# Kernel optimization log

Hardware: AMD Instinct MI355X
Metric: run time of the kernel (lower is better)

The kernel has to match this reference:

```python
import jax, jax.numpy as jnp
import numpy as np

N_NODES = 200000
N_EDGES = 6400000


def gcn_conv(x, src, dst, norm, num_nodes, W, b):
    # GCNConv: X' = D^{-1/2} (A+I) D^{-1/2} X W + b
    h = x @ W                                   # [N, out]
    msg = h[src] * norm[:, None]                # gather + scale per edge
    out = jax.ops.segment_sum(msg, dst, num_segments=num_nodes)
    return out + b


def build_norm(edge_index, num_nodes):
    # add self-loops, then symmetric normalization deg^{-1/2}[src]*deg^{-1/2}[dst]
    loops = jnp.arange(num_nodes, dtype=edge_index.dtype)
    src = jnp.concatenate([edge_index[0], loops])
    dst = jnp.concatenate([edge_index[1], loops])
    ones = jnp.ones(src.shape[0], dtype=jnp.float32)
    deg = jax.ops.segment_sum(ones, dst, num_segments=num_nodes)
    dinv = jnp.where(deg > 0, jax.lax.rsqrt(deg), 0.0)
    norm = dinv[src] * dinv[dst]
    return src, dst, norm


def setup_inputs() -> dict:
    key = jax.random.key(0)
    k1, k2, k3, k4 = jax.random.split(key, 4)
    x = jax.random.normal(k1, (N_NODES, 21), dtype=jnp.float32)
    edge_index = jax.random.randint(k2, (2, N_EDGES), 0, N_NODES, dtype=jnp.int64)
    W1 = jax.random.normal(k3, (21, 16), dtype=jnp.float32) * (1.0 / np.sqrt(21))
    b1 = jnp.zeros((16,), dtype=jnp.float32)
    W2 = jax.random.normal(k4, (16, 6), dtype=jnp.float32) * (1.0 / np.sqrt(16))
    b2 = jnp.zeros((6,), dtype=jnp.float32)
    return {"x": x, "edge_index": edge_index, "W1": W1, "b1": b1, "W2": W2, "b2": b2}


def reference(x, edge_index, W1, b1, W2, b2):
    num_nodes = x.shape[0]
    src, dst, norm = build_norm(edge_index, num_nodes)
    h = gcn_conv(x, src, dst, norm, num_nodes, W1, b1)
    h = jax.nn.relu(h)
    # F.dropout with training=self.training: eval mode -> identity
    h = gcn_conv(h, src, dst, norm, num_nodes, W2, b2)
    return jax.nn.log_softmax(h, axis=1)
```

## Files before the change

kernel.cpp:

```cpp
#include <hip/hip_runtime.h>
#include <hip/hip_fp16.h>

#define NFEAT_IN 21
#define NHID 16
#define NOUT 6
#define BSHIFT 9
#define BW (1 << BSHIFT)
#define NB 512
#define PB 256
#define EPT 32
#define CHUNK (PB * EPT)

typedef unsigned int u32x4 __attribute__((ext_vector_type(4)));

__global__ void k_init_bcur(int* __restrict__ bcur, int cap) {
    int b = blockIdx.x * blockDim.x + threadIdx.x;
    if (b < NB) bcur[b] = b * cap;
}

__global__ __launch_bounds__(256) void
k_partition(const int* __restrict__ src, const int* __restrict__ dst,
            int* __restrict__ bcur, unsigned int* __restrict__ bucketed,
            int cap, int ne) {
    __shared__ unsigned int ebd[CHUNK];
    __shared__ unsigned short sidx[CHUNK];
    __shared__ int lcnt[NB], lstart[NB], lcur[NB], lbase[NB];
    __shared__ int s[PB];
    __shared__ int sh_total;
    int t = threadIdx.x;
    long base = (long)blockIdx.x * CHUNK;
    for (int b = t; b < NB; b += PB) lcnt[b] = 0;
    __syncthreads();
#pragma unroll
    for (int k = 0; k < EPT; k++) {
        int idx = t + k * PB;
        long e = base + idx;
        unsigned int v = 0xFFFFFFFFu;
        if (e < ne) {
            int d = dst[e];
            v = (unsigned int)d;
            atomicAdd(&lcnt[d >> BSHIFT], 1);
        }
        ebd[idx] = v;
    }
    __syncthreads();
    int v0 = lcnt[2 * t], v1 = lcnt[2 * t + 1];
    int pair = v0 + v1;
    s[t] = pair;
    __syncthreads();
    for (int off = 1; off < PB; off <<= 1) {
        int tv = (t >= off) ? s[t - off] : 0;
        __syncthreads();
        s[t] += tv;
        __syncthreads();
    }
    int ex = s[t] - pair;
    lstart[2 * t] = ex;          lcur[2 * t] = ex;
    lstart[2 * t + 1] = ex + v0; lcur[2 * t + 1] = ex + v0;
    if (v0 > 0) lbase[2 * t]     = atomicAdd(&bcur[2 * t],     v0);
    if (v1 > 0) lbase[2 * t + 1] = atomicAdd(&bcur[2 * t + 1], v1);
    if (t == PB - 1) sh_total = s[PB - 1];
    __syncthreads();
#pragma unroll
    for (int k = 0; k < EPT; k++) {
        int idx = t + k * PB;
        unsigned int d = ebd[idx];
        if (d != 0xFFFFFFFFu) {
            int r = atomicAdd(&lcur[d >> BSHIFT], 1);
            sidx[r] = (unsigned short)idx;
        }
    }
    __syncthreads();
    int total = sh_total;
#pragma unroll
    for (int k = 0; k < EPT; k++) {
        int j = t + k * PB;
        if (j < total) {
            int idx = sidx[j];
            unsigned int d = ebd[idx];
            int b = d >> BSHIFT;
            long gpos = (long)lbase[b] + (j - lstart[b]);
            int s_ = src[base + idx];
            if (gpos < (long)(b + 1) * cap)
                bucketed[gpos] = ((unsigned int)s_ << BSHIFT) | (d & (BW - 1));
        }
    }
}

__global__ __launch_bounds__(512) void
k_cnt_scan(const int* __restrict__ bcur, int cap, int* __restrict__ cnt,
           int* __restrict__ csr_boff, int nb) {
    __shared__ int s[512];
    int t = threadIdx.x;
    int c = (t < nb) ? (bcur[t] - t * cap) : 0;
    s[t] = c;
    __syncthreads();
    for (int off = 1; off < 512; off <<= 1) {
        int tv = (t >= off) ? s[t - off] : 0;
        __syncthreads();
        s[t] += tv;
        __syncthreads();
    }
    if (t < nb) { cnt[t] = c; csr_boff[t] = s[t] - c; }
}

__global__ __launch_bounds__(512) void
k_sort(const unsigned int* __restrict__ bucketed, int cap,
       const int* __restrict__ cnt, const int* __restrict__ csr_boff,
       int* __restrict__ csr_src, int* __restrict__ node_off,
       float* __restrict__ dinv, int n, int ne, int nb) {
    __shared__ int bin[BW], sc[BW], bcur_l[BW];
    int b = blockIdx.x, t = threadIdx.x;
    bin[t] = 0;
    __syncthreads();
    size_t s0r = (size_t)b * cap;
    int c = cnt[b], s0c = csr_boff[b];
    for (int j = t; j < c; j += 512) atomicAdd(&bin[bucketed[s0r + j] & (BW - 1)], 1);
    __syncthreads();
    sc[t] = bin[t];
    __syncthreads();
    for (int off = 1; off < BW; off <<= 1) {
        int v = (t >= off) ? sc[t - off] : 0;
        __syncthreads();
        sc[t] += v;
        __syncthreads();
    }
    {
        int ex = sc[t] - bin[t];
        bcur_l[t] = s0c + ex;
        node_off[(b << BSHIFT) + t] = s0c + ex;
        int node = (b << BSHIFT) + t;
        if (node < n) dinv[node] = rsqrtf((float)bin[t] + 1.0f);
    }
    if (b == 0 && t == 0) node_off[(size_t)nb << BSHIFT] = ne;
    __syncthreads();
    for (int j = t; j < c; j += 512) {
        unsigned int e = bucketed[s0r + j];
        int pos = atomicAdd(&bcur_l[e & (BW - 1)], 1);
        csr_src[pos] = (int)(e >> BSHIFT);
    }
}

__global__ void k_dense1(const float* __restrict__ x, const float* __restrict__ W1,
                         const float* __restrict__ dinv, __half2* __restrict__ hs1h, int n) {
    __shared__ float sW[NFEAT_IN * NHID];
    for (int t = threadIdx.x; t < NFEAT_IN * NHID; t += blockDim.x) sW[t] = W1[t];
    __syncthreads();
    int i = blockIdx.x * blockDim.x + threadIdx.x;
    if (i >= n) return;
    float xi[NFEAT_IN];
#pragma unroll
    for (int k = 0; k < NFEAT_IN; k++) xi[k] = x[(size_t)i * NFEAT_IN + k];
    float di = dinv[i];
    float r[NHID];
#pragma unroll
    for (int j = 0; j < NHID; j++) {
        float acc = 0.f;
#pragma unroll
        for (int k = 0; k < NFEAT_IN; k++) acc += xi[k] * sW[k * NHID + j];
        r[j] = acc * di;
    }
    __half2* hp = hs1h + (size_t)i * 8;
#pragma unroll
    for (int q = 0; q < 8; q++) hp[q] = __floats2half2_rn(r[2 * q], r[2 * q + 1]);
}

__device__ __forceinline__ void addh16(float* acc, u32x4 u0, u32x4 u1) {
    unsigned int us[8] = {u0[0], u0[1], u0[2], u0[3], u1[0], u1[1], u1[2], u1[3]};
#pragma unroll
    for (int q = 0; q < 8; q++) {
        float2 f = __half22float2(*(const __half2*)&us[q]);
        acc[2 * q] += f.x;
        acc[2 * q + 1] += f.y;
    }
}

__global__ __launch_bounds__(256) void
k_agg1(const int* __restrict__ csr_src, const int* __restrict__ node_off,
       const __half2* __restrict__ hs1h, const float* __restrict__ b1,
       const float* __restrict__ W2, const float* __restrict__ dinv,
       __half2* __restrict__ hs2h, int n) {
    __shared__ float sW[NHID * NOUT];
    __shared__ float sb[NHID];
    int t = threadIdx.x;
    if (t < NHID * NOUT) sW[t] = W2[t];
    if (t < NHID) sb[t] = b1[t];
    __syncthreads();
    int i = blockIdx.x * blockDim.x + t;
    if (i >= n) return;
    int beg = node_off[i], end = node_off[i + 1];
    const u32x4* hb = (const u32x4*)hs1h;
    float acc[NHID];
    {
        u32x4 u0 = hb[(size_t)i * 2], u1 = hb[(size_t)i * 2 + 1];
        unsigned int us[8] = {u0[0], u0[1], u0[2], u0[3], u1[0], u1[1], u1[2], u1[3]};
#pragma unroll
        for (int q = 0; q < 8; q++) {
            float2 f = __half22float2(*(const __half2*)&us[q]);
            acc[2 * q] = f.x;
            acc[2 * q + 1] = f.y;
        }
    }
    int j = beg;
    for (; j + 4 <= end; j += 4) {
        int s0_ = csr_src[j], s1_ = csr_src[j + 1];
        int s2_ = csr_src[j + 2], s3_ = csr_src[j + 3];
        u32x4 a0 = hb[(size_t)s0_ * 2], a1 = hb[(size_t)s0_ * 2 + 1];
        u32x4 b0 = hb[(size_t)s1_ * 2], b1v = hb[(size_t)s1_ * 2 + 1];
        u32x4 c0 = hb[(size_t)s2_ * 2], c1 = hb[(size_t)s2_ * 2 + 1];
        u32x4 d0 = hb[(size_t)s3_ * 2], d1 = hb[(size_t)s3_ * 2 + 1];
        addh16(acc, a0, a1);
        addh16(acc, b0, b1v);
        addh16(acc, c0, c1);
        addh16(acc, d0, d1);
    }
    for (; j < end; j++) {
        int s_ = csr_src[j];
        addh16(acc, hb[(size_t)s_ * 2], hb[(size_t)s_ * 2 + 1]);
    }
    float di = dinv[i];
    float z[NHID];
#pragma unroll
    for (int k = 0; k < NHID; k++) z[k] = fmaxf(acc[k] * di + sb[k], 0.0f);
    float h[8];
#pragma unroll
    for (int kk = 0; kk < NOUT; kk++) {
        float s = 0.f;
#pragma unroll
        for (int jj = 0; jj < NHID; jj++) s += z[jj] * sW[jj * NOUT + kk];
        h[kk] = s * di;
    }
    h[6] = 0.f; h[7] = 0.f;
    __half2* op = hs2h + (size_t)i * 4;
#pragma unroll
    for (int q = 0; q < 4; q++) op[q] = __floats2half2_rn(h[2 * q], h[2 * q + 1]);
}

__global__ __launch_bounds__(256) void
k_agg2(const int* __restrict__ csr_src, const int* __restrict__ node_off,
       const __half2* __restrict__ hs2h, const float* __restrict__ b2,
       const float* __restrict__ dinv, float* __restrict__ out, int n) {
    __shared__ float sb[NOUT];
    int t = threadIdx.x;
    if (t < NOUT) sb[t] = b2[t];
    __syncthreads();
    int i = blockIdx.x * blockDim.x + t;
    if (i >= n) return;
    int beg = node_off[i], end = node_off[i + 1];
    const u32x4* hb = (const u32x4*)hs2h;
    float acc[NOUT];
    {
        u32x4 u = hb[(size_t)i];
        unsigned int us[3] = {u[0], u[1], u[2]};
#pragma unroll
        for (int q = 0; q < 3; q++) {
            float2 f = __half22float2(*(const __half2*)&us[q]);
            acc[2 * q] = f.x;
            acc[2 * q + 1] = f.y;
        }
    }
    int j = beg;
    for (; j + 8 <= end; j += 8) {
        int sid[8];
#pragma unroll
        for (int q = 0; q < 8; q++) sid[q] = csr_src[j + q];
        u32x4 u[8];
#pragma unroll
        for (int q = 0; q < 8; q++) u[q] = hb[(size_t)sid[q]];
#pragma unroll
        for (int q = 0; q < 8; q++) {
            unsigned int us[3] = {u[q][0], u[q][1], u[q][2]};
#pragma unroll
            for (int w = 0; w < 3; w++) {
                float2 fv = __half22float2(*(const __half2*)&us[w]);
                acc[2 * w] += fv.x;
                acc[2 * w + 1] += fv.y;
            }
        }
    }
    for (; j < end; j++) {
        u32x4 u = hb[(size_t)csr_src[j]];
        unsigned int us[3] = {u[0], u[1], u[2]};
#pragma unroll
        for (int w = 0; w < 3; w++) {
            float2 fv = __half22float2(*(const __half2*)&us[w]);
            acc[2 * w] += fv.x;
            acc[2 * w + 1] += fv.y;
        }
    }
    float di = dinv[i];
    float v[NOUT];
#pragma unroll
    for (int k = 0; k < NOUT; k++) v[k] = acc[k] * di + sb[k];
    float m = -1e30f;
#pragma unroll
    for (int k = 0; k < NOUT; k++) m = fmaxf(m, v[k]);
    float se = 0.f;
#pragma unroll
    for (int k = 0; k < NOUT; k++) se += expf(v[k] - m);
    float l = logf(se);
#pragma unroll
    for (int k = 0; k < NOUT; k++) out[(size_t)i * NOUT + k] = v[k] - m - l;
}

extern "C" void kernel_launch(void* const* d_in, const int* in_sizes, int n_in,
                              void* d_out, int out_size, void* d_ws, size_t ws_size,
                              hipStream_t stream) {
    const float* x  = (const float*)d_in[0];
    const int*   ei = (const int*)d_in[1];
    const float* W1 = (const float*)d_in[2];
    const float* b1 = (const float*)d_in[3];
    const float* W2 = (const float*)d_in[4];
    const float* b2 = (const float*)d_in[5];
    float* out = (float*)d_out;

    int n  = in_sizes[0] / NFEAT_IN;
    int ne = in_sizes[1] / 2;
    const int* src = ei;
    const int* dst = ei + ne;

    int nb = (n + BW - 1) >> BSHIFT;
    int cap = (ne + nb - 1) / nb + ne / (nb * 16) + 1536;

    char* base = (char*)d_ws;
    size_t off = 0;
    auto alloc = [&](size_t bytes) {
        void* p = base + off;
        off += (bytes + 63) & ~(size_t)63;
        return p;
    };
    int* bcur     = (int*)alloc(NB * 4);
    int* cnt      = (int*)alloc(NB * 4);
    int* csr_boff = (int*)alloc(NB * 4);
    unsigned int* bucketed = (unsigned int*)alloc((size_t)nb * cap * 4);
    int* csr_src  = (int*)alloc((size_t)ne * 4);
    int* node_off = (int*)alloc(((size_t)nb * BW + 1) * 4);
    float* dinv   = (float*)alloc((size_t)n * 4);
    __half2* hs1h;
    __half2* hs2h;
    if ((size_t)nb * cap * 4 >= (size_t)n * 48) {
        hs1h = (__half2*)bucketed;
        hs2h = (__half2*)((char*)bucketed + (size_t)n * 32);
    } else {
        hs1h = (__half2*)alloc((size_t)n * 32);
        hs2h = (__half2*)alloc((size_t)n * 16);
    }

    int gp = (ne + CHUNK - 1) / CHUNK;
    int gn = (n + 255) / 256;

    k_init_bcur<<<(NB + 255) / 256, 256, 0, stream>>>(bcur, cap);
    k_partition<<<gp, PB, 0, stream>>>(src, dst, bcur, bucketed, cap, ne);
    k_cnt_scan<<<1, 512, 0, stream>>>(bcur, cap, cnt, csr_boff, nb);
    k_sort<<<nb, 512, 0, stream>>>(bucketed, cap, cnt, csr_boff, csr_src, node_off, dinv, n, ne, nb);
    k_dense1<<<gn, 256, 0, stream>>>(x, W1, dinv, hs1h, n);
    k_agg1<<<gn, 256, 0, stream>>>(csr_src, node_off, hs1h, b1, W2, dinv, hs2h, n);
    k_agg2<<<gn, 256, 0, stream>>>(csr_src, node_off, hs2h, b2, dinv, out, n);
}
```

Baseline: 399.5 us.

## Split layer-1 aggregation into two feature-half passes over separate fp16 arrays

The hidden features are stored as two separate 8-wide fp16 arrays (low and high halves), and layer-1 aggregation becomes two kernels, each gathering one 16-byte half per edge. The first pass writes fp32 partial sums, which the second pass reads and combines. The idea is to halve the working set of each gather (3.2MB per half) so it stays cache-resident and random gathers hit more often. The cost is reading the CSR twice, an extra partial-sum round trip and one more launch; CSR index loads are also marked nontemporal.

```diff
diff --git a/kernel.cpp b/kernel.cpp
--- a/kernel.cpp
+++ b/kernel.cpp
@@ -142,7 +142,9 @@
 }
 
 __global__ void k_dense1(const float* __restrict__ x, const float* __restrict__ W1,
-                         const float* __restrict__ dinv, __half2* __restrict__ hs1h, int n) {
+                         const float* __restrict__ dinv,
+                         __half2* __restrict__ hs1lo, __half2* __restrict__ hs1hi,
+                         int n) {
     __shared__ float sW[NFEAT_IN * NHID];
     for (int t = threadIdx.x; t < NFEAT_IN * NHID; t += blockDim.x) sW[t] = W1[t];
     __syncthreads();
@@ -160,15 +162,19 @@
         for (int k = 0; k < NFEAT_IN; k++) acc += xi[k] * sW[k * NHID + j];
         r[j] = acc * di;
     }
-    __half2* hp = hs1h + (size_t)i * 8;
-#pragma unroll
-    for (int q = 0; q < 8; q++) hp[q] = __floats2half2_rn(r[2 * q], r[2 * q + 1]);
-}
-
-__device__ __forceinline__ void addh16(float* acc, u32x4 u0, u32x4 u1) {
-    unsigned int us[8] = {u0[0], u0[1], u0[2], u0[3], u1[0], u1[1], u1[2], u1[3]};
-#pragma unroll
-    for (int q = 0; q < 8; q++) {
+    __half2* lp = hs1lo + (size_t)i * 4;
+    __half2* hp = hs1hi + (size_t)i * 4;
+#pragma unroll
+    for (int q = 0; q < 4; q++) {
+        lp[q] = __floats2half2_rn(r[2 * q], r[2 * q + 1]);
+        hp[q] = __floats2half2_rn(r[8 + 2 * q], r[8 + 2 * q + 1]);
+    }
+}
+
+__device__ __forceinline__ void addh8(float* acc, u32x4 u) {
+    unsigned int us[4] = {u[0], u[1], u[2], u[3]};
+#pragma unroll
+    for (int q = 0; q < 4; q++) {
         float2 f = __half22float2(*(const __half2*)&us[q]);
         acc[2 * q] += f.x;
         acc[2 * q + 1] += f.y;
@@ -176,10 +182,44 @@
 }
 
 __global__ __launch_bounds__(256) void
-k_agg1(const int* __restrict__ csr_src, const int* __restrict__ node_off,
-       const __half2* __restrict__ hs1h, const float* __restrict__ b1,
-       const float* __restrict__ W2, const float* __restrict__ dinv,
-       __half2* __restrict__ hs2h, int n) {
+k_agg1a(const int* __restrict__ csr_src, const int* __restrict__ node_off,
+        const u32x4* __restrict__ hlo, float* __restrict__ pacc, int n) {
+    int i = blockIdx.x * blockDim.x + threadIdx.x;
+    if (i >= n) return;
+    int beg = node_off[i], end = node_off[i + 1];
+    float acc[8];
+    {
+        u32x4 u = hlo[i];
+        unsigned int us[4] = {u[0], u[1], u[2], u[3]};
+#pragma unroll
+        for (int q = 0; q < 4; q++) {
+            float2 f = __half22float2(*(const __half2*)&us[q]);
+            acc[2 * q] = f.x;
+            acc[2 * q + 1] = f.y;
+        }
+    }
+    int j = beg;
+    for (; j + 8 <= end; j += 8) {
+        int sid[8];
+#pragma unroll
+        for (int q = 0; q < 8; q++) sid[q] = __builtin_nontemporal_load(csr_src + j + q);
+        u32x4 u[8];
+#pragma unroll
+        for (int q = 0; q < 8; q++) u[q] = hlo[(size_t)sid[q]];
+#pragma unroll
+        for (int q = 0; q < 8; q++) addh8(acc, u[q]);
+    }
+    for (; j < end; j++) addh8(acc, hlo[(size_t)csr_src[j]]);
+    float4* pp = (float4*)(pacc + (size_t)i * 8);
+    pp[0] = make_float4(acc[0], acc[1], acc[2], acc[3]);
+    pp[1] = make_float4(acc[4], acc[5], acc[6], acc[7]);
+}
+
+__global__ __launch_bounds__(256) void
+k_agg1b(const int* __restrict__ csr_src, const int* __restrict__ node_off,
+        const u32x4* __restrict__ hhi, const float* __restrict__ pacc,
+        const float* __restrict__ b1, const float* __restrict__ W2,
+        const float* __restrict__ dinv, __half2* __restrict__ hs2h, int n) {
     __shared__ float sW[NHID * NOUT];
     __shared__ float sb[NHID];
     int t = threadIdx.x;
@@ -189,39 +229,43 @@
     int i = blockIdx.x * blockDim.x + t;
     if (i >= n) return;
     int beg = node_off[i], end = node_off[i + 1];
-    const u32x4* hb = (const u32x4*)hs1h;
-    float acc[NHID];
+    float acc[8];
     {
-        u32x4 u0 = hb[(size_t)i * 2], u1 = hb[(size_t)i * 2 + 1];
-        unsigned int us[8] = {u0[0], u0[1], u0[2], u0[3], u1[0], u1[1], u1[2], u1[3]};
-#pragma unroll
-        for (int q = 0; q < 8; q++) {
+        u32x4 u = hhi[i];
+        unsigned int us[4] = {u[0], u[1], u[2], u[3]};
+#pragma unroll
+        for (int q = 0; q < 4; q++) {
             float2 f = __half22float2(*(const __half2*)&us[q]);
             acc[2 * q] = f.x;
             acc[2 * q + 1] = f.y;
         }
     }
     int j = beg;
-    for (; j + 4 <= end; j += 4) {
-        int s0_ = csr_src[j], s1_ = csr_src[j + 1];
-        int s2_ = csr_src[j + 2], s3_ = csr_src[j + 3];
-        u32x4 a0 = hb[(size_t)s0_ * 2], a1 = hb[(size_t)s0_ * 2 + 1];
-        u32x4 b0 = hb[(size_t)s1_ * 2], b1v = hb[(size_t)s1_ * 2 + 1];
-        u32x4 c0 = hb[(size_t)s2_ * 2], c1 = hb[(size_t)s2_ * 2 + 1];
-        u32x4 d0 = hb[(size_t)s3_ * 2], d1 = hb[(size_t)s3_ * 2 + 1];
-        addh16(acc, a0, a1);
-        addh16(acc, b0, b1v);
-        addh16(acc, c0, c1);
-        addh16(acc, d0, d1);
-    }
-    for (; j < end; j++) {
-        int s_ = csr_src[j];
-        addh16(acc, hb[(size_t)s_ * 2], hb[(size_t)s_ * 2 + 1]);
-    }
+    for (; j + 8 <= end; j += 8) {
+        int sid[8];
+#pragma unroll
+        for (int q = 0; q < 8; q++) sid[q] = __builtin_nontemporal_load(csr_src + j + q);
+        u32x4 u[8];
+#pragma unroll
+        for (int q = 0; q < 8; q++) u[q] = hhi[(size_t)sid[q]];
+#pragma unroll
+        for (int q = 0; q < 8; q++) addh8(acc, u[q]);
+    }
+    for (; j < end; j++) addh8(acc, hhi[(size_t)csr_src[j]]);
+    const float4* pp = (const float4*)(pacc + (size_t)i * 8);
+    float4 p0 = pp[0], p1 = pp[1];
     float di = dinv[i];
     float z[NHID];
-#pragma unroll
-    for (int k = 0; k < NHID; k++) z[k] = fmaxf(acc[k] * di + sb[k], 0.0f);
+    z[0] = fmaxf(p0.x * di + sb[0], 0.0f);
+    z[1] = fmaxf(p0.y * di + sb[1], 0.0f);
+    z[2] = fmaxf(p0.z * di + sb[2], 0.0f);
+    z[3] = fmaxf(p0.w * di + sb[3], 0.0f);
+    z[4] = fmaxf(p1.x * di + sb[4], 0.0f);
+    z[5] = fmaxf(p1.y * di + sb[5], 0.0f);
+    z[6] = fmaxf(p1.z * di + sb[6], 0.0f);
+    z[7] = fmaxf(p1.w * di + sb[7], 0.0f);
+#pragma unroll
+    for (int k = 0; k < 8; k++) z[8 + k] = fmaxf(acc[k] * di + sb[8 + k], 0.0f);
     float h[8];
 #pragma unroll
     for (int kk = 0; kk < NOUT; kk++) {
@@ -263,7 +307,7 @@
     for (; j + 8 <= end; j += 8) {
         int sid[8];
 #pragma unroll
-        for (int q = 0; q < 8; q++) sid[q] = csr_src[j + q];
+        for (int q = 0; q < 8; q++) sid[q] = __builtin_nontemporal_load(csr_src + j + q);
         u32x4 u[8];
 #pragma unroll
         for (int q = 0; q < 8; q++) u[q] = hb[(size_t)sid[q]];
@@ -336,14 +380,18 @@
     int* csr_src  = (int*)alloc((size_t)ne * 4);
     int* node_off = (int*)alloc(((size_t)nb * BW + 1) * 4);
     float* dinv   = (float*)alloc((size_t)n * 4);
-    __half2* hs1h;
-    __half2* hs2h;
-    if ((size_t)nb * cap * 4 >= (size_t)n * 48) {
-        hs1h = (__half2*)bucketed;
-        hs2h = (__half2*)((char*)bucketed + (size_t)n * 32);
+    __half2 *hs1lo, *hs1hi, *hs2h;
+    float* pacc;
+    if ((size_t)nb * cap * 4 >= (size_t)n * 80) {
+        hs1lo = (__half2*)bucketed;
+        hs1hi = (__half2*)((char*)bucketed + (size_t)n * 16);
+        hs2h  = (__half2*)((char*)bucketed + (size_t)n * 32);
+        pacc  = (float*)((char*)bucketed + (size_t)n * 48);
     } else {
-        hs1h = (__half2*)alloc((size_t)n * 32);
-        hs2h = (__half2*)alloc((size_t)n * 16);
+        hs1lo = (__half2*)alloc((size_t)n * 16);
+        hs1hi = (__half2*)alloc((size_t)n * 16);
+        hs2h  = (__half2*)alloc((size_t)n * 16);
+        pacc  = (float*)alloc((size_t)n * 32);
     }
 
     int gp = (ne + CHUNK - 1) / CHUNK;
@@ -353,7 +401,8 @@
     k_partition<<<gp, PB, 0, stream>>>(src, dst, bcur, bucketed, cap, ne);
     k_cnt_scan<<<1, 512, 0, stream>>>(bcur, cap, cnt, csr_boff, nb);
     k_sort<<<nb, 512, 0, stream>>>(bucketed, cap, cnt, csr_boff, csr_src, node_off, dinv, n, ne, nb);
-    k_dense1<<<gn, 256, 0, stream>>>(x, W1, dinv, hs1h, n);
-    k_agg1<<<gn, 256, 0, stream>>>(csr_src, node_off, hs1h, b1, W2, dinv, hs2h, n);
+    k_dense1<<<gn, 256, 0, stream>>>(x, W1, dinv, hs1lo, hs1hi, n);
+    k_agg1a<<<gn, 256, 0, stream>>>(csr_src, node_off, (const u32x4*)hs1lo, pacc, n);
+    k_agg1b<<<gn, 256, 0, stream>>>(csr_src, node_off, (const u32x4*)hs1hi, pacc, b1, W2, dinv, hs2h, n);
     k_agg2<<<gn, 256, 0, stream>>>(csr_src, node_off, hs2h, b2, dinv, out, n);
 }
```

Measured after the change: 440.6 us. 1.1x slower.
